# Kernel optimization log

Hardware: AMD Instinct MI355X
Metric: run time of the kernel (lower is better)

## Reference

```python
import jax, jax.numpy as jnp
import numpy as np
from jax import lax

S = 224          # raster_settings.image_size
K = 10           # raster_settings.faces_per_pixel
BLUR = 1e-4      # raster_settings.blur_radius (signed squared-dist threshold)
SIGMA = 1e-4     # BlendParams().sigma used by sigmoid_alpha_blend
BIG = 1e10
AREA_EPS = 1e-10


def setup_inputs():
    key = jax.random.key(0)
    k1, k2, k3 = jax.random.split(key, 3)
    B, V, F = 2, 5023, 5000
    xy = jax.random.uniform(k1, (B, V, 2), minval=-1.0, maxval=1.0)
    z = jax.random.uniform(k2, (B, V, 1), minval=0.5, maxval=1.5)
    vertices = jnp.concatenate([xy, z], -1).astype(jnp.float32)
    faces = jax.random.randint(k3, (B, F, 3), 0, V, dtype=jnp.int32)
    return {"vertices": vertices, "faces": faces}


def _cross2(a, b):
    return a[..., 0] * b[..., 1] - a[..., 1] * b[..., 0]


def _edge_d2(a, b, p):
    # squared distance from points p [W,1,2] to segment (a,b) [F,2] -> [W,F]
    ab = b - a
    ap = p - a
    t = jnp.clip((ap * ab).sum(-1) / jnp.maximum((ab * ab).sum(-1), 1e-12), 0.0, 1.0)
    proj = a + t[..., None] * ab
    return ((p - proj) ** 2).sum(-1)


def _rasterize_one(verts, faces):
    # naive PyTorch3D-style rasterizer for one mesh: per pixel, keep K nearest
    # faces (by interpolated z) whose signed squared dist to the triangle < BLUR.
    tri = verts[faces]                                  # [F,3,3]
    v0, v1, v2 = tri[:, 0, :2], tri[:, 1, :2], tri[:, 2, :2]
    z0, z1, z2 = tri[:, 0, 2], tri[:, 1, 2], tri[:, 2, 2]
    area = _cross2(v1 - v0, v2 - v0)
    good_face = jnp.abs(area) > AREA_EPS                # cull degenerate faces
    area_safe = jnp.where(good_face, area, 1.0)
    # NDC pixel centers (pytorch3d convention: +x left, +y up; verts pre-negated)
    coords = 1.0 - (2.0 * jnp.arange(S, dtype=verts.dtype) + 1.0) / S

    def row(yf):
        p = jnp.stack([coords, jnp.full((S,), yf, verts.dtype)], -1)[:, None, :]  # [W,1,2]
        w0 = _cross2(v2 - v1, p - v1) / area_safe       # [W,F] barycentric
        w1 = _cross2(v0 - v2, p - v2) / area_safe
        w2 = _cross2(v1 - v0, p - v0) / area_safe
        z = w0 * z0 + w1 * z1 + w2 * z2                  # no perspective correction (default)
        inside = (w0 > 0) & (w1 > 0) & (w2 > 0)
        d2 = jnp.minimum(jnp.minimum(_edge_d2(v0, v1, p), _edge_d2(v1, v2, p)),
                         _edge_d2(v2, v0, p))
        sd = jnp.where(inside, -d2, d2)                  # signed squared dist
        valid = good_face & (z > 0) & (sd <= BLUR)
        negz = jnp.where(valid, -z, -BIG)
        vals, idx = lax.top_k(negz, K)                   # K nearest by z
        vk = vals > -0.5 * BIG
        zk = jnp.take_along_axis(z, idx, -1)
        dk = jnp.take_along_axis(sd, idx, -1)
        return (jnp.where(vk, idx, -1), jnp.where(vk, zk, -1.0), jnp.where(vk, dk, -1.0))

    return lax.map(row, coords)                          # each [S,S,K]


def reference(vertices, faces):
    B, V, _ = vertices.shape
    F = faces.shape[1]
    fixed = vertices * jnp.array([-1.0, -1.0, 1.0], vertices.dtype)  # flip x,y (DECA)
    p2f_l, zbuf, dists = jax.vmap(_rasterize_one)(fixed, faces)      # [B,S,S,K]
    mask = p2f_l >= 0
    # packed (global) pix_to_face like pytorch3d
    p2f = jnp.where(mask, p2f_l + (jnp.arange(B) * F)[:, None, None, None], -1)
    # sigmoid_alpha_blend: alpha = 1 - prod(1 - sigmoid(-dist/sigma))
    prob = jax.nn.sigmoid(-dists / SIGMA) * mask
    alpha = 1.0 - jnp.prod(1.0 - prob, -1)               # [B,S,S]
    images = alpha[:, None, :, :]                        # images[...,3:].permute(0,3,1,2)
    # vertex visibility from nearest face per pixel (scatter)
    faces_packed = (faces + V * jnp.arange(B, dtype=faces.dtype)[:, None, None]).reshape(-1, 3)
    faces_all = jnp.concatenate([faces_packed, -jnp.ones((1, 3), faces.dtype)], 0)
    vis_verts = faces_all[p2f[..., 0].reshape(-1)].reshape(-1)  # -1 wraps to sentinel row
    vv = jnp.zeros(B * V + 1, vertices.dtype).at[vis_verts].set(1.0)
    visibility = vv[:-1].reshape(B, V)                   # extra slot absorbs -1 indices
    return images, visibility
```

## Files before the change

kernel.cpp:

```cpp
#include <hip/hip_runtime.h>
#include <math.h>

#define SDIM 224
#define KTOP 10
#define NB 2
#define NV 5023
#define NF 5000
#define BLUR 1e-4f
#define IMG_SZ (NB * SDIM * SDIM)
#define NW 8
#define SEG (NF / NW)
#define CAP 1536
#define HT 0.031251f
#define COV_THR 0.04422f
#define REL_THR (-0.0543f)

__device__ __forceinline__ float seg_d2_exact(float ax, float ay, float abx, float aby,
                                              float L, float px, float py) {
    float apx = __fsub_rn(px, ax), apy = __fsub_rn(py, ay);
    float dot = __fadd_rn(__fmul_rn(apx, abx), __fmul_rn(apy, aby));
    float t = __fdiv_rn(dot, L);
    t = fminf(fmaxf(t, 0.0f), 1.0f);
    float prx = __fadd_rn(ax, __fmul_rn(t, abx));
    float pry = __fadd_rn(ay, __fmul_rn(t, aby));
    float dx = __fsub_rn(px, prx), dy = __fsub_rn(py, pry);
    return __fadd_rn(__fmul_rn(dx, dx), __fmul_rn(dy, dy));
}

__global__ void preprocess_kernel(const float* __restrict__ verts,
                                  const int* __restrict__ faces,
                                  float4* __restrict__ ga,
                                  float4* __restrict__ hh,
                                  float4* __restrict__ cc,
                                  float* __restrict__ out)
{
    const int idx = blockIdx.x * blockDim.x + threadIdx.x;
    if (idx < NB * NV) out[IMG_SZ + idx] = 0.0f;
    if (idx >= NB * NF) return;
    const int b = idx / NF;
    const int* fp = faces + (size_t)idx * 3;
    const int i0 = fp[0], i1 = fp[1], i2 = fp[2];
    const float* vb = verts + (size_t)b * NV * 3;
    const float v0x = -vb[i0*3+0], v0y = -vb[i0*3+1], z0 = vb[i0*3+2];
    const float v1x = -vb[i1*3+0], v1y = -vb[i1*3+1], z1 = vb[i1*3+2];
    const float v2x = -vb[i2*3+0], v2y = -vb[i2*3+1], z2 = vb[i2*3+2];
    const float e01x = __fsub_rn(v1x, v0x), e01y = __fsub_rn(v1y, v0y);
    const float e12x = __fsub_rn(v2x, v1x), e12y = __fsub_rn(v2y, v1y);
    const float e20x = __fsub_rn(v0x, v2x), e20y = __fsub_rn(v0y, v2y);
    const float area = __fsub_rn(__fmul_rn(e01x, __fsub_rn(v2y, v0y)),
                                 __fmul_rn(e01y, __fsub_rn(v2x, v0x)));
    const bool good = fabsf(area) > 1e-10f;
    const float area_safe = good ? area : 1.0f;

    double Zx = 0.0, Zy = 0.0, Zc = 0.0;
    float mgc = -1.0f;
    float n0x=0,n0y=0,n0c=-3e38f, n1x=0,n1y=0,n1c=-3e38f, n2x=0,n2y=0,n2c=-3e38f;
    float zloF = 3e38f, zhiF = -1.0f;
    if (good) {
        const double invA = 1.0 / (double)area;
        const double c0c = (double)e12y*v1x - (double)e12x*v1y;
        const double c1c = (double)e20y*v2x - (double)e20x*v2y;
        const double c2c = (double)e01y*v0x - (double)e01x*v0y;
        Zx = (-(double)e12y*z0 - (double)e20y*z1 - (double)e01y*z2) * invA;
        Zy = ( (double)e12x*z0 + (double)e20x*z1 + (double)e01x*z2) * invA;
        Zc = (c0c*z0 + c1c*z1 + c2c*z2) * invA;
        const double B0 = fabs((double)e12x)*(1.0+fabs((double)v1y)) + fabs((double)e12y)*(1.0+fabs((double)v1x));
        const double B1 = fabs((double)e20x)*(1.0+fabs((double)v2y)) + fabs((double)e20y)*(1.0+fabs((double)v2x));
        const double B2 = fabs((double)e01x)*(1.0+fabs((double)v0y)) + fabs((double)e01y)*(1.0+fabs((double)v0x));
        const double B = (B0*(double)z0 + B1*(double)z1 + B2*(double)z2) * fabs(invA);
        mgc = (float)(2.5e-6 * B) + 1e-20f;
        const double s = (area > 0.0f) ? 1.0 : -1.0;
        const double l12 = sqrt((double)e12x*e12x + (double)e12y*e12y);
        const double l20 = sqrt((double)e20x*e20x + (double)e20y*e20y);
        const double l01 = sqrt((double)e01x*e01x + (double)e01y*e01y);
        const double i12 = s / fmax(l12, 1e-300);
        const double i20 = s / fmax(l20, 1e-300);
        const double i01 = s / fmax(l01, 1e-300);
        n0x = (float)(-(double)e12y * i12);
        n0y = (float)( (double)e12x * i12);
        n0c = (float)(((double)e12y*v1x - (double)e12x*v1y) * i12);
        n1x = (float)(-(double)e20y * i20);
        n1y = (float)( (double)e20x * i20);
        n1c = (float)(((double)e20y*v2x - (double)e20x*v2y) * i20);
        n2x = (float)(-(double)e01y * i01);
        n2y = (float)( (double)e01x * i01);
        n2c = (float)(((double)e01y*v0x - (double)e01x*v0y) * i01);
        const double gradZ = sqrt(Zx*Zx + Zy*Zy);
        const double zminV = fmin((double)z0, fmin((double)z1, (double)z2));
        const double zmaxV = fmax((double)z0, fmax((double)z1, (double)z2));
        zloF = (float)(zminV - 0.0102 * gradZ - (double)mgc - 1e-6);
        const bool elig = (zminV - (double)mgc - 1e-6) > 0.0;
        zhiF = elig ? (float)(zmaxV + (double)mgc + 1e-6) : -1.0f;
    }
    ga[idx]     = make_float4((float)Zx, (float)Zy, (float)Zc, mgc);
    cc[3*idx+0] = make_float4(n0x, n0y, n0c, n1x);
    cc[3*idx+1] = make_float4(n1y, n1c, n2x, n2y);
    cc[3*idx+2] = make_float4(n2c, zloF, zhiF, 0.0f);
    hh[3*idx+0] = make_float4(v0x, v0y, v1x, v1y);
    hh[3*idx+1] = make_float4(v2x, v2y, z0, z1);
    hh[3*idx+2] = make_float4(z2, area_safe, 0.0f, 0.0f);
}

__device__ __forceinline__ void heavy_face(float4 h0, float4 h1, float4 h2,
                                           int fidx, bool pass, float px, float py,
                                           float tz[KTOP], float ts[KTOP],
                                           float& bestZ, int& bestIdx)
{
    if (!pass) return;
    const float v0x=h0.x, v0y=h0.y, v1x=h0.z, v1y=h0.w;
    const float v2x=h1.x, v2y=h1.y, z0=h1.z, z1=h1.w;
    const float z2=h2.x, area=h2.y;
    const float e01x = __fsub_rn(v1x, v0x), e01y = __fsub_rn(v1y, v0y);
    const float e12x = __fsub_rn(v2x, v1x), e12y = __fsub_rn(v2y, v1y);
    const float e20x = __fsub_rn(v0x, v2x), e20y = __fsub_rn(v0y, v2y);

    const float c0 = __fsub_rn(__fmul_rn(e12x, __fsub_rn(py, v1y)),
                               __fmul_rn(e12y, __fsub_rn(px, v1x)));
    const float c1 = __fsub_rn(__fmul_rn(e20x, __fsub_rn(py, v2y)),
                               __fmul_rn(e20y, __fsub_rn(px, v2x)));
    const float c2 = __fsub_rn(__fmul_rn(e01x, __fsub_rn(py, v0y)),
                               __fmul_rn(e01y, __fsub_rn(px, v0x)));

    const float L01 = fmaxf(__fadd_rn(__fmul_rn(e01x,e01x), __fmul_rn(e01y,e01y)), 1e-12f);
    const float L12 = fmaxf(__fadd_rn(__fmul_rn(e12x,e12x), __fmul_rn(e12y,e12y)), 1e-12f);
    const float L20 = fmaxf(__fadd_rn(__fmul_rn(e20x,e20x), __fmul_rn(e20y,e20y)), 1e-12f);

    const bool ap = area > 0.0f;
    const bool s0 = ap ? (c0 > 0.0f) : (c0 < 0.0f);
    const bool s1 = ap ? (c1 > 0.0f) : (c1 < 0.0f);
    const bool s2 = ap ? (c2 > 0.0f) : (c2 < 0.0f);
    if (!(s0 & s1 & s2)) {
        bool cull = false;
        if (!s0) cull |= (c0 * c0 > BLUR * 1.0002f * L12);
        if (!s1) cull |= (c1 * c1 > BLUR * 1.0002f * L20);
        if (!s2) cull |= (c2 * c2 > BLUR * 1.0002f * L01);
        if (cull) return;
    }

    const float w0 = __fdiv_rn(c0, area);
    const float w1 = __fdiv_rn(c1, area);
    const float w2 = __fdiv_rn(c2, area);
    const float z = __fadd_rn(__fadd_rn(__fmul_rn(w0, z0), __fmul_rn(w1, z1)),
                              __fmul_rn(w2, z2));
    if (!(z > 0.0f)) return;
    if (!(z < tz[KTOP-1])) return;

    const bool inside = (w0 > 0.0f) & (w1 > 0.0f) & (w2 > 0.0f);
    float sd;
    if (inside) {
        const bool sat = (c0*c0 >= 1.0002e-3f * L12) &
                         (c1*c1 >= 1.0002e-3f * L20) &
                         (c2*c2 >= 1.0002e-3f * L01);
        if (sat) {
            sd = -1.0f;
        } else {
            const float d2 = fminf(fminf(
                seg_d2_exact(v0x, v0y, e01x, e01y, L01, px, py),
                seg_d2_exact(v1x, v1y, e12x, e12y, L12, px, py)),
                seg_d2_exact(v2x, v2y, e20x, e20y, L20, px, py));
            sd = -d2;
        }
    } else {
        const float d2 = fminf(fminf(
            seg_d2_exact(v0x, v0y, e01x, e01y, L01, px, py),
            seg_d2_exact(v1x, v1y, e12x, e12y, L12, px, py)),
            seg_d2_exact(v2x, v2y, e20x, e20y, L20, px, py));
        if (!(d2 <= BLUR)) return;
        sd = d2;
    }

    if (z < bestZ) { bestZ = z; bestIdx = fidx; }

    float cz = z, cs = sd;
#pragma unroll
    for (int j = 0; j < KTOP; ++j) {
        if (cz < tz[j]) {
            const float oz = tz[j], os = ts[j];
            tz[j] = cz; ts[j] = cs; cz = oz; cs = os;
        }
    }
}

__global__ __launch_bounds__(64 * NW) void raster_kernel(const float4* __restrict__ gaG,
                                                         const float4* __restrict__ hhG,
                                                         const float4* __restrict__ ccG,
                                                         const int* __restrict__ faces,
                                                         float* __restrict__ out)
{
    const int b = blockIdx.z;
    const int lane = threadIdx.x & 63;
    const int w = __builtin_amdgcn_readfirstlane((int)(threadIdx.x >> 6));
    const int x = (blockIdx.x << 3) + (lane & 7);
    const int y = (blockIdx.y << 3) + (lane >> 3);
    const float px = __fsub_rn(1.0f, __fdiv_rn(__fadd_rn(__fmul_rn(2.0f, (float)x), 1.0f), (float)SDIM));
    const float py = __fsub_rn(1.0f, __fdiv_rn(__fadd_rn(__fmul_rn(2.0f, (float)y), 1.0f), (float)SDIM));
    const float pcx = __fsub_rn(1.0f, __fdiv_rn((float)(16 * blockIdx.x + 8), 224.0f));
    const float pcy = __fsub_rn(1.0f, __fdiv_rn((float)(16 * blockIdx.y + 8), 224.0f));

    __shared__ int   sList[CAP];
    __shared__ int   sHist[64];
    __shared__ int   sCnt[NW];
    __shared__ int   sOff[NW];
    __shared__ int   sLen;
    __shared__ float sT;
    __shared__ float sZ[NW][64][11];
    __shared__ float sS[NW][64][11];
    __shared__ int   sBI[NW][64];

    if (threadIdx.x < 64) sHist[threadIdx.x] = 0;
    __syncthreads();

    const float4* __restrict__ ga = gaG + (size_t)b * NF;
    const float4* __restrict__ hh = hhG + (size_t)b * NF * 3;
    const float4* __restrict__ cc = ccG + (size_t)b * NF * 3;

    const int f0 = w * SEG, f1 = f0 + SEG;
    float dm[10], zl[10];
#pragma unroll
    for (int it = 0; it < 10; ++it) {
        const int f = f0 + it * 64 + lane;
        dm[it] = -3e38f; zl[it] = 3e38f;
        if (f < f1) {
            const float4 a0 = ga[f];
            const float4 cA = cc[3*f+0];
            const float4 cB = cc[3*f+1];
            const float4 cC = cc[3*f+2];
            const float d0 = fmaf(cA.x, pcx, fmaf(cA.y, pcy, cA.z));
            const float d1 = fmaf(cA.w, pcx, fmaf(cB.x, pcy, cB.y));
            const float d2 = fmaf(cB.z, pcx, fmaf(cB.w, pcy, cC.x));
            const float dmin = fminf(d0, fminf(d1, d2));
            const float ztc = fmaf(a0.x, pcx, fmaf(a0.y, pcy, a0.z));
            const float spread = fmaf(fabsf(a0.x), HT, fmaf(fabsf(a0.y), HT, 2.0f * fabsf(a0.w))) + 1e-6f;
            dm[it] = dmin;
            zl[it] = fmaxf(ztc - spread, cC.y);
            if ((cC.z > 0.0f) && (dmin >= COV_THR)) {
                const float zh = fminf(ztc + spread, cC.z);
                int bk = (int)floorf((zh - 0.4f) * 53.333332f);
                bk = max(0, min(63, bk));
                atomicAdd(&sHist[bk], 1);
            }
        }
    }
    __syncthreads();

    if (threadIdx.x == 0) {
        int cum = 0; float T = 3e38f;
        for (int k2 = 0; k2 < 64; ++k2) {
            cum += sHist[k2];
            if (cum >= KTOP) { T = (k2 >= 63) ? 3e38f : (0.4f + (float)(k2+1) * 0.01875f + 1e-4f); break; }
        }
        sT = T;
    }
    __syncthreads();
    const float Tt = sT;

    int svMask = 0, cnt = 0;
#pragma unroll
    for (int it = 0; it < 10; ++it) {
        const bool sv = (dm[it] >= REL_THR) && (zl[it] <= Tt);
        if (sv) svMask |= (1 << it);
        cnt += (int)__popcll(__ballot(sv));
    }
    if (lane == 0) sCnt[w] = cnt;
    __syncthreads();
    if (threadIdx.x == 0) {
        int acc = 0;
        for (int w2 = 0; w2 < NW; ++w2) { sOff[w2] = acc; acc += sCnt[w2]; }
        sLen = (acc <= CAP) ? acc : -1;
    }
    __syncthreads();
    const int Ltot = sLen;

    if (Ltot >= 0) {
        const unsigned long long below = ((lane == 63) ? ~0ull : ((1ull << (lane + 1)) - 1ull)) >> 1;
        int woff = sOff[w];
#pragma unroll
        for (int it = 0; it < 10; ++it) {
            const bool sv = (svMask >> it) & 1;
            const unsigned long long m = __ballot(sv);
            if (sv) sList[woff + (int)__popcll(m & below)] = f0 + it * 64 + lane;
            woff += (int)__popcll(m);
        }
    }
    __syncthreads();

    float tz[KTOP], ts[KTOP];
#pragma unroll
    for (int j = 0; j < KTOP; ++j) { tz[j] = 3e38f; ts[j] = 3e38f; }
    float bestZ = 3e38f;
    int bestIdx = -1;

    if (Ltot >= 0) {
        const int chunk = (Ltot + NW - 1) / NW;
        const int jb = w * chunk, je = min(Ltot, jb + chunk);
        for (int j = jb; j < je; ++j) {
            const int f = __builtin_amdgcn_readfirstlane(sList[j]);
            const float4 g = ga[f];
            const float zt  = fmaf(g.x, px, fmaf(g.y, py, g.z));
            const float thr = fminf(tz[KTOP-1], Tt);
            const bool pass = (zt > -g.w) & (zt < thr + g.w);
            if (__any(pass)) {
                heavy_face(hh[3*f+0], hh[3*f+1], hh[3*f+2], f, pass, px, py,
                           tz, ts, bestZ, bestIdx);
            }
        }
    } else {
        for (int f = f0; f < f1; ++f) {
            const float4 g = ga[f];
            const float zt  = fmaf(g.x, px, fmaf(g.y, py, g.z));
            const float thr = fminf(tz[KTOP-1], Tt);
            const bool pass = (zt > -g.w) & (zt < thr + g.w);
            if (__any(pass)) {
                heavy_face(hh[3*f+0], hh[3*f+1], hh[3*f+2], f, pass, px, py,
                           tz, ts, bestZ, bestIdx);
            }
        }
    }

#pragma unroll
    for (int j = 0; j < KTOP; ++j) { sZ[w][lane][j] = tz[j]; sS[w][lane][j] = ts[j]; }
    sZ[w][lane][KTOP] = 3e38f;
    sBI[w][lane] = bestIdx;
    __syncthreads();

    if (threadIdx.x < 64) {
        const int p = threadIdx.x;
        float bz = sZ[0][p][0]; int bi = sBI[0][p];
#pragma unroll
        for (int w2 = 1; w2 < NW; ++w2) {
            const float zc = sZ[w2][p][0];
            if (zc < bz) { bz = zc; bi = sBI[w2][p]; }
        }
        int ptr[NW];
#pragma unroll
        for (int w2 = 0; w2 < NW; ++w2) ptr[w2] = 0;
        float prod = 1.0f;
#pragma unroll
        for (int k = 0; k < KTOP; ++k) {
            float mz = 3e38f; int mw = -1;
#pragma unroll
            for (int w2 = 0; w2 < NW; ++w2) {
                const float zc = sZ[w2][p][ptr[w2]];
                if (zc < mz) { mz = zc; mw = w2; }
            }
            float sd = 3e38f;
#pragma unroll
            for (int w2 = 0; w2 < NW; ++w2) {
                if (w2 == mw) { sd = sS[w2][p][ptr[w2]]; ptr[w2]++; }
            }
            prod *= 1.0f / (1.0f + __expf(-sd * 1e4f));
        }
        const float alpha = 1.0f - prod;
        const int gx = (blockIdx.x << 3) + (p & 7);
        const int gy = (blockIdx.y << 3) + (p >> 3);
        out[(size_t)b * (SDIM * SDIM) + gy * SDIM + gx] = alpha;

        if (bi >= 0) {
            const int* fp = faces + ((size_t)b * NF + bi) * 3;
            float* vis = out + IMG_SZ;
            vis[b * NV + fp[0]] = 1.0f;
            vis[b * NV + fp[1]] = 1.0f;
            vis[b * NV + fp[2]] = 1.0f;
        }
    }
}

extern "C" void kernel_launch(void* const* d_in, const int* in_sizes, int n_in,
                              void* d_out, int out_size, void* d_ws, size_t ws_size,
                              hipStream_t stream)
{
    const float* verts = (const float*)d_in[0];
    const int*   faces = (const int*)d_in[1];
    float* out = (float*)d_out;
    float4* ga = (float4*)d_ws;
    float4* hh = (float4*)((char*)d_ws + NB * NF * 16);
    float4* cc = (float4*)((char*)d_ws + NB * NF * (16 + 48));

    const int total = NB * NV;
    preprocess_kernel<<<dim3((total + 255) / 256), dim3(256), 0, stream>>>(verts, faces, ga, hh, cc, out);
    raster_kernel<<<dim3(SDIM / 8, SDIM / 8, NB), dim3(64 * NW), 0, stream>>>(ga, hh, cc, faces, out);
}
```

Before: 187.5 us.

## Compact per-pixel candidate faces into LDS queues before heavy rasterization

Adds a pre-pass in which each lane tests every listed face against its own pixel, using depth bounds plus edge-function distances. Passing face indices go into a per-lane LDS queue of up to 20 entries, and the heavy per-face test then iterates only over each lane's own queue. This cuts wave divergence, where whole waves ran heavy_face for faces only a few lanes needed. If any queue overflows, the block falls back to the old path. The change also shrinks the list capacity and adds a launch-bounds occupancy hint, at the cost of an extra pass over the list and gathered, non-uniform loads of face data.

```diff
diff --git a/kernel.cpp b/kernel.cpp
--- a/kernel.cpp
+++ b/kernel.cpp
@@ -10,7 +10,8 @@
 #define IMG_SZ (NB * SDIM * SDIM)
 #define NW 8
 #define SEG (NF / NW)
-#define CAP 1536
+#define CAP 1024
+#define Q1 20
 #define HT 0.031251f
 #define COV_THR 0.04422f
 #define REL_THR (-0.0543f)
@@ -181,11 +182,11 @@
     }
 }
 
-__global__ __launch_bounds__(64 * NW) void raster_kernel(const float4* __restrict__ gaG,
-                                                         const float4* __restrict__ hhG,
-                                                         const float4* __restrict__ ccG,
-                                                         const int* __restrict__ faces,
-                                                         float* __restrict__ out)
+__global__ __launch_bounds__(64 * NW, 6) void raster_kernel(const float4* __restrict__ gaG,
+                                                            const float4* __restrict__ hhG,
+                                                            const float4* __restrict__ ccG,
+                                                            const int* __restrict__ faces,
+                                                            float* __restrict__ out)
 {
     const int b = blockIdx.z;
     const int lane = threadIdx.x & 63;
@@ -198,16 +199,19 @@
     const float pcy = __fsub_rn(1.0f, __fdiv_rn((float)(16 * blockIdx.y + 8), 224.0f));
 
     __shared__ int   sList[CAP];
+    __shared__ unsigned short sQ[NW * Q1 * 64];
     __shared__ int   sHist[64];
     __shared__ int   sCnt[NW];
     __shared__ int   sOff[NW];
     __shared__ int   sLen;
+    __shared__ int   sOvf;
     __shared__ float sT;
     __shared__ float sZ[NW][64][11];
     __shared__ float sS[NW][64][11];
     __shared__ int   sBI[NW][64];
 
     if (threadIdx.x < 64) sHist[threadIdx.x] = 0;
+    if (threadIdx.x == 0) sOvf = 0;
     __syncthreads();
 
     const float4* __restrict__ ga = gaG + (size_t)b * NF;
@@ -254,14 +258,14 @@
     __syncthreads();
     const float Tt = sT;
 
-    int svMask = 0, cnt = 0;
+    int svMask = 0, cnt1 = 0;
 #pragma unroll
     for (int it = 0; it < 10; ++it) {
         const bool sv = (dm[it] >= REL_THR) && (zl[it] <= Tt);
         if (sv) svMask |= (1 << it);
-        cnt += (int)__popcll(__ballot(sv));
-    }
-    if (lane == 0) sCnt[w] = cnt;
+        cnt1 += (int)__popcll(__ballot(sv));
+    }
+    if (lane == 0) sCnt[w] = cnt1;
     __syncthreads();
     if (threadIdx.x == 0) {
         int acc = 0;
@@ -290,9 +294,42 @@
     float bestZ = 3e38f;
     int bestIdx = -1;
 
+    int qn = 0;
+    int jb = 0, je = 0;
     if (Ltot >= 0) {
         const int chunk = (Ltot + NW - 1) / NW;
-        const int jb = w * chunk, je = min(Ltot, jb + chunk);
+        jb = w * chunk; je = min(Ltot, jb + chunk);
+        for (int j = jb; j < je; ++j) {
+            const int f = __builtin_amdgcn_readfirstlane(sList[j]);
+            const float4 g = ga[f];
+            const float4 cA = cc[3*f+0];
+            const float4 cB = cc[3*f+1];
+            const float4 cC = cc[3*f+2];
+            const float zt = fmaf(g.x, px, fmaf(g.y, py, g.z));
+            const float d0 = fmaf(cA.x, px, fmaf(cA.y, py, cA.z));
+            const float d1 = fmaf(cA.w, px, fmaf(cB.x, py, cB.y));
+            const float d2 = fmaf(cB.z, px, fmaf(cB.w, py, cC.x));
+            const float dmin = fminf(d0, fminf(d1, d2));
+            const bool pass = (zt > -g.w) & (zt < Tt + g.w) & (dmin >= -0.0102f);
+            if (pass) {
+                if (qn < Q1) { sQ[(w * Q1 + qn) * 64 + lane] = (unsigned short)f; qn++; }
+                else atomicOr(&sOvf, 1);
+            }
+        }
+    }
+    __syncthreads();
+    const int ovf = sOvf;
+
+    if (Ltot >= 0 && !ovf) {
+        for (int i = 0; __any(i < qn); ++i) {
+            const bool act = (i < qn);
+            const int f = act ? (int)sQ[(w * Q1 + i) * 64 + lane] : 0;
+            const float4 h0 = hh[3*f+0];
+            const float4 h1 = hh[3*f+1];
+            const float4 h2 = hh[3*f+2];
+            heavy_face(h0, h1, h2, f, act, px, py, tz, ts, bestZ, bestIdx);
+        }
+    } else if (Ltot >= 0) {
         for (int j = jb; j < je; ++j) {
             const int f = __builtin_amdgcn_readfirstlane(sList[j]);
             const float4 g = ga[f];
```

Result: no change. 190.9 us (+1.8%).
